# Optimization experiments

Hardware: AMD Instinct MI355X
Metric: run time of the kernel (lower is better)

The kernel has to match this reference:

```python
import jax, jax.numpy as jnp
import numpy as np

TAU = 0.05
EPS = 1e-5
NHEAD = 4

def _ln(x, s, b):
    m = jnp.mean(x, -1, keepdims=True)
    v = jnp.mean((x - m) ** 2, -1, keepdims=True)
    return (x - m) * jax.lax.rsqrt(v + EPS) * s + b

def _encoder(z, mask, w_qkv, b_qkv, w_o, b_o, w_ff1, b_ff1, w_ff2, b_ff2, ln1_s, ln1_b, ln2_s, ln2_b):
    # z: [B,L,D], mask: [B,L] bool, True = padded (masked out of attention)
    B, L, D = z.shape
    H = NHEAD
    hd = D // H
    scale = 1.0 / float(np.sqrt(hd))
    nlayers = w_qkv.shape[0]
    for l in range(nlayers):
        qkv = z @ w_qkv[l].T + b_qkv[l]              # [B,L,3D]
        q, k, v = jnp.split(qkv, 3, axis=-1)
        q = q.reshape(B, L, H, hd).transpose(0, 2, 1, 3)  # [B,H,L,hd]
        k = k.reshape(B, L, H, hd).transpose(0, 2, 1, 3)
        v = v.reshape(B, L, H, hd).transpose(0, 2, 1, 3)
        scores = jnp.einsum('bhqd,bhkd->bhqk', q, k) * scale
        scores = jnp.where(mask[:, None, None, :], -1e9, scores)
        attn = jax.nn.softmax(scores, axis=-1)
        o = jnp.einsum('bhqk,bhkd->bhqd', attn, v).transpose(0, 2, 1, 3).reshape(B, L, D)
        z = _ln(z + o @ w_o[l].T + b_o[l], ln1_s[l], ln1_b[l])
        ff = jax.nn.relu(z @ w_ff1[l].T + b_ff1[l]) @ w_ff2[l].T + b_ff2[l]
        z = _ln(z + ff, ln2_s[l], ln2_b[l])
    return z

def _branch(x, mask, w0, b0, enc_p, w1, b1, w2, b2):
    base = x[..., None] * w0[:, 0] + b0          # Linear(1, latent) on [B,L,1]
    enc = _encoder(base, mask, *enc_p)
    h = jnp.mean(enc, axis=1)                    # mean over seq (incl. padded, as original)
    h = jnp.tanh(h @ w1.T + b1)
    return jnp.tanh(h @ w2.T + b2)


def setup_inputs() -> dict:
    key = jax.random.key(0)
    B, L, D, FF, NL, C = 256, 256, 128, 2048, 3, 3
    ks = jax.random.split(key, 16)
    w = lambda k, shape: jax.random.normal(k, shape, jnp.float32) * 0.02
    return {
        'x': jax.random.normal(ks[0], (B, L), jnp.float32),
        'x_pos': jax.random.normal(ks[1], (B, L), jnp.float32),
        'x_neg': jax.random.normal(ks[2], (B, L), jnp.float32),
        'mask': jnp.zeros((B, L), bool),
        'pos_mask': jnp.zeros((B, L), bool),
        'neg_mask': jnp.zeros((B, L), bool),
        'w0': w(ks[3], (D, 1)), 'b0': jnp.zeros((D,), jnp.float32),
        'w_qkv': w(ks[4], (NL, 3 * D, D)), 'b_qkv': jnp.zeros((NL, 3 * D), jnp.float32),
        'w_o': w(ks[5], (NL, D, D)), 'b_o': jnp.zeros((NL, D), jnp.float32),
        'w_ff1': w(ks[6], (NL, FF, D)), 'b_ff1': jnp.zeros((NL, FF), jnp.float32),
        'w_ff2': w(ks[7], (NL, D, FF)), 'b_ff2': jnp.zeros((NL, D), jnp.float32),
        'ln1_s': jnp.ones((NL, D), jnp.float32), 'ln1_b': jnp.zeros((NL, D), jnp.float32),
        'ln2_s': jnp.ones((NL, D), jnp.float32), 'ln2_b': jnp.zeros((NL, D), jnp.float32),
        'w1': w(ks[8], (D, D)), 'b1': jnp.zeros((D,), jnp.float32),
        'w2': w(ks[9], (D, D)), 'b2': jnp.zeros((D,), jnp.float32),
        'w3': w(ks[10], (C, D)), 'b3': jnp.zeros((C,), jnp.float32),
    }


def reference(x, x_pos, x_neg, mask, pos_mask, neg_mask, w0, b0, w_qkv, b_qkv, w_o, b_o,
              w_ff1, b_ff1, w_ff2, b_ff2, ln1_s, ln1_b, ln2_s, ln2_b, w1, b1, w2, b2, w3, b3):
    enc_p = (w_qkv, b_qkv, w_o, b_o, w_ff1, b_ff1, w_ff2, b_ff2, ln1_s, ln1_b, ln2_s, ln2_b)
    hb = _branch(x, mask, w0, b0, enc_p, w1, b1, w2, b2)        # [B,D]
    hp = _branch(x_pos, pos_mask, w0, b0, enc_p, w1, b1, w2, b2)
    hn = _branch(x_neg, neg_mask, w0, b0, enc_p, w1, b1, w2, b2)
    logits = jax.nn.softmax(hb @ w3.T + b3, axis=1)
    nb = hb / jnp.linalg.norm(hb, axis=1, keepdims=True)
    nps = hp / jnp.linalg.norm(hp, axis=1, keepdims=True)
    nns = hn / jnp.linalg.norm(hn, axis=1, keepdims=True)
    # InfoNCE: bottom_i = sum_j exp(<nb_i,np_j>/tau) + exp(<nb_i,nn_j>/tau)
    pos_sim = jnp.sum(nb * nps, axis=1) / TAU                   # diag of nb@nps.T
    S = jnp.concatenate([nb @ nps.T, nb @ nns.T], axis=1) / TAU  # [B,2B]
    loss = jnp.mean(jax.nn.logsumexp(S, axis=1) - pos_sim)
    return (nb, hp, hn, logits, loss)
```

## Files before the change

kernel.cpp:

```cpp
#include <hip/hip_runtime.h>
#include <stdint.h>

typedef unsigned short u16;
typedef unsigned int   u32;
typedef unsigned long long u64;
typedef __bf16 bf16x8 __attribute__((ext_vector_type(8)));
typedef __bf16 bf16x4t __attribute__((ext_vector_type(4)));
typedef float  f32x4  __attribute__((ext_vector_type(4)));

#define LN_EPS 1e-5f
#define LSEQ   256
#define DM     128
#define B3     768
#define MTOT   196608
#define NQKV   384
#define FFD    2048

__device__ __forceinline__ u16 f2bf(float f) {
  __bf16 h = (__bf16)f;
  return __builtin_bit_cast(u16, h);
}
__device__ __forceinline__ float bf2f(u16 h) {
  u32 u = ((u32)h) << 16;
  return __builtin_bit_cast(float, u);
}
__device__ __forceinline__ bf16x8 ld_bf8(const u16* p) {
  return __builtin_bit_cast(bf16x8, *(const uint4*)p);
}
__device__ __forceinline__ f32x4 mfma16(bf16x8 a, bf16x8 b, f32x4 c) {
  return __builtin_amdgcn_mfma_f32_16x16x32_bf16(a, b, c, 0, 0, 0);
}
__device__ __forceinline__ void gload16(const u16* g, u16* l) {
  __builtin_amdgcn_global_load_lds(
      (__attribute__((address_space(1))) void*)(uintptr_t)g,
      (__attribute__((address_space(3))) void*)(uintptr_t)l, 16, 0, 0);
}
__device__ __forceinline__ u64 pack4bf(float a, float b, float c, float d) {
  bf16x4t t;
  t[0] = (__bf16)a; t[1] = (__bf16)b; t[2] = (__bf16)c; t[3] = (__bf16)d;
  return __builtin_bit_cast(u64, t);
}

__global__ __launch_bounds__(256) void k_cvt(const float* src, u16* dst, int n8) {
  int gid = blockIdx.x * 256 + threadIdx.x;
  if (gid >= n8) return;
  const float* s = src + gid * 8;
  union { u16 o[8]; uint4 v; } t;
#pragma unroll
  for (int j = 0; j < 8; ++j) t.o[j] = f2bf(s[j]);
  *(uint4*)(dst + (size_t)gid * 8) = t.v;
}

__global__ __launch_bounds__(256) void k_embed(const float* x, const float* xp, const float* xn,
                                               const float* w0, const float* b0, u16* zb) {
  int gid = blockIdx.x * 256 + threadIdx.x;
  int row = gid >> 4;
  int oct = gid & 15;
  int br  = row >> 16;
  int loc = row & 65535;
  const float* xs = br == 0 ? x : (br == 1 ? xp : xn);
  float xv = xs[loc];
  int d0 = oct * 8;
  union { u16 o[8]; uint4 v; } t;
#pragma unroll
  for (int j = 0; j < 8; ++j) t.o[j] = f2bf(xv * w0[d0 + j] + b0[d0 + j]);
  *(uint4*)(zb + (size_t)row * DM + d0) = t.v;
}

__global__ __launch_bounds__(256) void k_qkv(const u16* zb, const u16* wt, const float* bias, u16* out) {
  __shared__ union {
    struct { u16 A[16384]; u16 B[16384]; } s;
    u16 bounce[128 * 136];
  } u;
  int tid = threadIdx.x;
  int m0 = blockIdx.x * 128;
  int n0 = blockIdx.y * 128;
#pragma unroll
  for (int p = 0; p < 8; ++p) {
    int row = p * 16 + (tid >> 4);
    int gs = (tid & 15) ^ (row & 7);
    gload16(wt + (u64)(n0 + row) * 128 + gs * 8, u.s.A + p * 2048 + tid * 8);
  }
#pragma unroll
  for (int p = 0; p < 8; ++p) {
    int row = p * 16 + (tid >> 4);
    int gs = (tid & 15) ^ (row & 7);
    gload16(zb + (u64)(m0 + row) * 128 + gs * 8, u.s.B + p * 2048 + tid * 8);
  }
  __syncthreads();

  int lane = tid & 63, wv = tid >> 6;
  int l15 = lane & 15, g = lane >> 4;
  int wn = wv & 1, wm = wv >> 1;
  f32x4 acc[4][4] = {};
#pragma unroll
  for (int ks = 0; ks < 4; ++ks) {
    bf16x8 a[4], b[4];
#pragma unroll
    for (int i = 0; i < 4; ++i) {
      int row = wn * 64 + i * 16 + l15;
      int gz = (ks * 4 + g) ^ (row & 7);
      a[i] = ld_bf8(u.s.A + row * 128 + gz * 8);
    }
#pragma unroll
    for (int j = 0; j < 4; ++j) {
      int row = wm * 64 + j * 16 + l15;
      int gz = (ks * 4 + g) ^ (row & 7);
      b[j] = ld_bf8(u.s.B + row * 128 + gz * 8);
    }
#pragma unroll
    for (int i = 0; i < 4; ++i)
#pragma unroll
      for (int j = 0; j < 4; ++j) acc[i][j] = mfma16(a[i], b[j], acc[i][j]);
  }
  float bv[4][4];
#pragma unroll
  for (int i = 0; i < 4; ++i)
    *(f32x4*)bv[i] = *(const f32x4*)(bias + n0 + wn * 64 + i * 16 + g * 4);
  __syncthreads();
#pragma unroll
  for (int i = 0; i < 4; ++i) {
    int nq = wn * 64 + i * 16 + g * 4;
#pragma unroll
    for (int j = 0; j < 4; ++j) {
      int m = wm * 64 + j * 16 + l15;
      u64 pk = pack4bf(acc[i][j][0] + bv[i][0], acc[i][j][1] + bv[i][1],
                       acc[i][j][2] + bv[i][2], acc[i][j][3] + bv[i][3]);
      *(u64*)(u.bounce + m * 136 + nq) = pk;
    }
  }
  __syncthreads();
  {
    int row = tid >> 1, half = tid & 1;
    const u16* src = u.bounce + row * 136 + half * 64;
    u16* dst = out + (u64)(m0 + row) * NQKV + n0 + half * 64;
#pragma unroll
    for (int q = 0; q < 8; ++q) *(uint4*)(dst + q * 8) = *(const uint4*)(src + q * 8);
  }
}

__global__ __launch_bounds__(256) void k_attn(const u16* qkv, const unsigned char* mk0,
                                              const unsigned char* mk1, const unsigned char* mk2,
                                              u16* attno) {
  __shared__ u16 VT[32 * 264];
  __shared__ u16 P[4][64 * 72];
  __shared__ float pen[256];
  int tid = threadIdx.x;
  int bh = blockIdx.x;
  int bb = bh >> 2, h = bh & 3;
  {
    int br = bb >> 8, loc = bb & 255;
    const unsigned char* mp = br == 0 ? mk0 : (br == 1 ? mk1 : mk2);
    pen[tid] = mp[loc * 256 + tid] ? -1e9f : 0.0f;
  }
  {
    const u16* vsrc = qkv + (u64)(bb * 256 + tid) * NQKV + 256 + h * 32;
    u16 tmp[32];
    *(uint4*)(tmp) = *(const uint4*)vsrc;
    *(uint4*)(tmp + 8) = *(const uint4*)(vsrc + 8);
    *(uint4*)(tmp + 16) = *(const uint4*)(vsrc + 16);
    *(uint4*)(tmp + 24) = *(const uint4*)(vsrc + 24);
#pragma unroll
    for (int d = 0; d < 32; ++d) VT[d * 264 + tid] = tmp[d];
  }
  __syncthreads();

  int lane = tid & 63, wv = tid >> 6;
  int l15 = lane & 15, g = lane >> 4;
  const float scale2 = 0.25503492149314874f;

  bf16x8 qf[4];
#pragma unroll
  for (int j = 0; j < 4; ++j)
    qf[j] = ld_bf8(qkv + (u64)(bb * 256 + wv * 64 + j * 16 + l15) * NQKV + h * 32 + g * 8);
  bf16x8 kf[16];
#pragma unroll
  for (int kb = 0; kb < 16; ++kb)
    kf[kb] = ld_bf8(qkv + (u64)(bb * 256 + kb * 16 + l15) * NQKV + 128 + h * 32 + g * 8);

  f32x4 accO[2][4] = {};
  float lpart[4] = {0.f, 0.f, 0.f, 0.f};
  u16* Pw = &P[wv][0];
  f32x4 zf = {0.f, 0.f, 0.f, 0.f};

#pragma unroll
  for (int t = 0; t < 4; ++t) {
    f32x4 pq[4];
#pragma unroll
    for (int i = 0; i < 4; ++i) pq[i] = *(const f32x4*)(pen + t * 64 + i * 16 + g * 4);
#pragma unroll
    for (int jq = 0; jq < 4; ++jq) {
      f32x4 s[4];
#pragma unroll
      for (int i = 0; i < 4; ++i) s[i] = mfma16(kf[t * 4 + i], qf[jq], zf);
#pragma unroll
      for (int i = 0; i < 4; ++i) {
        float p0 = __builtin_amdgcn_exp2f(fmaf(s[i][0], scale2, pq[i][0]));
        float p1 = __builtin_amdgcn_exp2f(fmaf(s[i][1], scale2, pq[i][1]));
        float p2 = __builtin_amdgcn_exp2f(fmaf(s[i][2], scale2, pq[i][2]));
        float p3 = __builtin_amdgcn_exp2f(fmaf(s[i][3], scale2, pq[i][3]));
        lpart[jq] += (p0 + p1) + (p2 + p3);
        *(u64*)(Pw + (jq * 16 + l15) * 72 + i * 16 + g * 4) = pack4bf(p0, p1, p2, p3);
      }
    }
#pragma unroll
    for (int ks = 0; ks < 2; ++ks) {
      bf16x8 va[2], pb[4];
#pragma unroll
      for (int i = 0; i < 2; ++i)
        va[i] = ld_bf8(VT + (i * 16 + l15) * 264 + t * 64 + ks * 32 + g * 8);
#pragma unroll
      for (int jq = 0; jq < 4; ++jq)
        pb[jq] = ld_bf8(Pw + (jq * 16 + l15) * 72 + ks * 32 + g * 8);
#pragma unroll
      for (int i = 0; i < 2; ++i)
#pragma unroll
        for (int jq = 0; jq < 4; ++jq) accO[i][jq] = mfma16(va[i], pb[jq], accO[i][jq]);
    }
  }
#pragma unroll
  for (int jq = 0; jq < 4; ++jq) {
    float v = lpart[jq];
    v += __shfl_xor(v, 16);
    v += __shfl_xor(v, 32);
    lpart[jq] = 1.0f / v;
  }
#pragma unroll
  for (int i = 0; i < 2; ++i)
#pragma unroll
    for (int jq = 0; jq < 4; ++jq) {
      int q = wv * 64 + jq * 16 + l15;
      float li = lpart[jq];
      u64 pk = pack4bf(accO[i][jq][0] * li, accO[i][jq][1] * li,
                       accO[i][jq][2] * li, accO[i][jq][3] * li);
      *(u64*)(attno + ((u64)(bb * 4 + h) * 256 + q) * 32 + i * 16 + g * 4) = pk;
    }
}

__global__ __launch_bounds__(256) void k_oln(const u16* attno, const u16* wt, const float* bias,
                                             const float* lns, const float* lnb, u16* zb) {
  __shared__ union {
    struct { u16 A[16384]; u16 B[16384]; } s;
    float bounce[64 * 132];
  } u;
  int tid = threadIdx.x;
  int m0 = blockIdx.x * 128;
#pragma unroll
  for (int p = 0; p < 8; ++p) {
    int row = p * 16 + (tid >> 4);
    int gs = (tid & 15) ^ (row & 7);
    gload16(wt + (u64)row * 128 + gs * 8, u.s.A + p * 2048 + tid * 8);
  }
  int bb = m0 >> 8, lbase = m0 & 255;
#pragma unroll
  for (int p = 0; p < 8; ++p) {
    int row = p * 16 + (tid >> 4);
    int gs = (tid & 15) ^ (row & 7);
    int hh = gs >> 2, off = (gs & 3) * 8;
    gload16(attno + ((u64)(bb * 4 + hh) * 256 + lbase + row) * 32 + off,
            u.s.B + p * 2048 + tid * 8);
  }
  __syncthreads();

  int lane = tid & 63, wv = tid >> 6;
  int l15 = lane & 15, g = lane >> 4;
  int wn = wv & 1, wm = wv >> 1;
  f32x4 acc[4][4] = {};
#pragma unroll
  for (int ks = 0; ks < 4; ++ks) {
    bf16x8 a[4], b[4];
#pragma unroll
    for (int i = 0; i < 4; ++i) {
      int row = wn * 64 + i * 16 + l15;
      int gz = (ks * 4 + g) ^ (row & 7);
      a[i] = ld_bf8(u.s.A + row * 128 + gz * 8);
    }
#pragma unroll
    for (int j = 0; j < 4; ++j) {
      int row = wm * 64 + j * 16 + l15;
      int gz = (ks * 4 + g) ^ (row & 7);
      b[j] = ld_bf8(u.s.B + row * 128 + gz * 8);
    }
#pragma unroll
    for (int i = 0; i < 4; ++i)
#pragma unroll
      for (int j = 0; j < 4; ++j) acc[i][j] = mfma16(a[i], b[j], acc[i][j]);
  }
  for (int ph = 0; ph < 2; ++ph) {
    __syncthreads();
    if (wm == ph) {
#pragma unroll
      for (int i = 0; i < 4; ++i)
#pragma unroll
        for (int j = 0; j < 4; ++j) {
          int ml = j * 16 + l15;
          int nq = wn * 64 + i * 16 + g * 4;
          *(f32x4*)(u.bounce + ml * 132 + nq) = acc[i][j];
        }
    }
    __syncthreads();
    {
      int ql = tid >> 2, q4 = tid & 3;
      int mrow = m0 + ph * 64 + ql;
      const u16* zrow = zb + (u64)mrow * 128 + q4 * 32;
      float v[32];
      float s = 0.f, s2 = 0.f;
#pragma unroll
      for (int c = 0; c < 32; ++c) {
        float val = u.bounce[ql * 132 + q4 * 32 + c] + bias[q4 * 32 + c] + bf2f(zrow[c]);
        v[c] = val; s += val; s2 += val * val;
      }
      s += __shfl_xor(s, 1);  s += __shfl_xor(s, 2);
      s2 += __shfl_xor(s2, 1); s2 += __shfl_xor(s2, 2);
      float mean = s * (1.0f / 128.0f);
      float var = s2 * (1.0f / 128.0f) - mean * mean;
      float rstd = rsqrtf(var + LN_EPS);
      union { u16 o[32]; uint4 q[4]; } t;
#pragma unroll
      for (int c = 0; c < 32; ++c)
        t.o[c] = f2bf((v[c] - mean) * rstd * lns[q4 * 32 + c] + lnb[q4 * 32 + c]);
      u16* dst = zb + (u64)mrow * 128 + q4 * 32;
#pragma unroll
      for (int q = 0; q < 4; ++q) *(uint4*)(dst + q * 8) = t.q[q];
    }
  }
}

__global__ __launch_bounds__(256, 2) void k_ffn(u16* zb, const u16* w1, const float* b1,
                                                const u16* w2, const float* b2,
                                                const float* lns, const float* lnb) {
  __shared__ u16 W1b[2][8192];
  __shared__ u16 W2b[2][8192];
  __shared__ u16 H1s[4][2048];
  int tid = threadIdx.x;
  int m0 = blockIdx.x * 128;
  int lane = tid & 63, wv = tid >> 6;
  int l15 = lane & 15, g = lane >> 4;
  int qb = m0 + wv * 32;

  bf16x8 az[2][4];
#pragma unroll
  for (int j = 0; j < 2; ++j)
#pragma unroll
    for (int ks = 0; ks < 4; ++ks)
      az[j][ks] = ld_bf8(zb + (u64)(qb + j * 16 + l15) * 128 + ks * 32 + g * 8);

  {
#pragma unroll
    for (int p = 0; p < 4; ++p) {
      int row = p * 16 + (tid >> 4);
      int gs = (tid & 15) ^ (row & 7);
      gload16(w1 + (u64)row * 128 + gs * 8, W1b[0] + p * 2048 + tid * 8);
    }
#pragma unroll
    for (int p = 0; p < 4; ++p) {
      int row = p * 32 + (tid >> 3);
      int gs = (tid & 7) ^ (row & 7);
      gload16(w2 + (u64)row * FFD + gs * 8, W2b[0] + p * 2048 + tid * 8);
    }
  }
  __syncthreads();

  f32x4 acc2[8][2] = {};
  char* Hw = (char*)&H1s[wv][0];

  for (int c = 0; c < 32; ++c) {
    int cur = c & 1;
    if (c < 31) {
      const u16* w1n = w1 + (u64)(c + 1) * 64 * 128;
      const u16* w2n = w2 + (u64)(c + 1) * 64;
      u16* d1 = W1b[cur ^ 1];
      u16* d2 = W2b[cur ^ 1];
#pragma unroll
      for (int p = 0; p < 4; ++p) {
        int row = p * 16 + (tid >> 4);
        int gs = (tid & 15) ^ (row & 7);
        gload16(w1n + (u64)row * 128 + gs * 8, d1 + p * 2048 + tid * 8);
      }
#pragma unroll
      for (int p = 0; p < 4; ++p) {
        int row = p * 32 + (tid >> 3);
        int gs = (tid & 7) ^ (row & 7);
        gload16(w2n + (u64)row * FFD + gs * 8, d2 + p * 2048 + tid * 8);
      }
    }
    const u16* W1c = W1b[cur];
    const u16* W2c = W2b[cur];

    f32x4 a1[4][2] = {};
#pragma unroll
    for (int ks = 0; ks < 4; ++ks) {
      bf16x8 af[4];
#pragma unroll
      for (int i = 0; i < 4; ++i) {
        int row = i * 16 + l15;
        int gz = (ks * 4 + g) ^ (row & 7);
        af[i] = ld_bf8(W1c + row * 128 + gz * 8);
      }
#pragma unroll
      for (int i = 0; i < 4; ++i)
#pragma unroll
        for (int j = 0; j < 2; ++j) a1[i][j] = mfma16(af[i], az[j][ks], a1[i][j]);
    }
#pragma unroll
    for (int i = 0; i < 4; ++i) {
      f32x4 bq = *(const f32x4*)(b1 + c * 64 + i * 16 + g * 4);
#pragma unroll
      for (int j = 0; j < 2; ++j) {
        int q = j * 16 + l15;
        float t0 = a1[i][j][0] + bq[0]; t0 = t0 > 0.f ? t0 : 0.f;
        float t1 = a1[i][j][1] + bq[1]; t1 = t1 > 0.f ? t1 : 0.f;
        float t2 = a1[i][j][2] + bq[2]; t2 = t2 > 0.f ? t2 : 0.f;
        float t3 = a1[i][j][3] + bq[3]; t3 = t3 > 0.f ? t3 : 0.f;
        int off = (q * 128 + i * 32 + g * 8) ^ ((q & 7) << 4);
        *(u64*)(Hw + off) = pack4bf(t0, t1, t2, t3);
      }
    }
#pragma unroll
    for (int ks = 0; ks < 2; ++ks) {
      bf16x8 pb[2];
#pragma unroll
      for (int j = 0; j < 2; ++j) {
        int q = j * 16 + l15;
        int off = (q * 128 + ks * 64 + g * 16) ^ ((q & 7) << 4);
        pb[j] = ld_bf8((const u16*)(Hw + off));
      }
#pragma unroll
      for (int i = 0; i < 8; ++i) {
        int row = i * 16 + l15;
        int gz = (ks * 4 + g) ^ (row & 7);
        bf16x8 wf = ld_bf8(W2c + row * 64 + gz * 8);
#pragma unroll
        for (int j = 0; j < 2; ++j) acc2[i][j] = mfma16(wf, pb[j], acc2[i][j]);
      }
    }
    __syncthreads();
  }

  float s[2] = {0.f, 0.f}, s2[2] = {0.f, 0.f};
#pragma unroll
  for (int i = 0; i < 8; ++i) {
    f32x4 bq = *(const f32x4*)(b2 + i * 16 + g * 4);
#pragma unroll
    for (int j = 0; j < 2; ++j) {
      int q = qb + j * 16 + l15;
      u64 zo = *(const u64*)(zb + (u64)q * 128 + i * 16 + g * 4);
#pragma unroll
      for (int r = 0; r < 4; ++r) {
        float val = acc2[i][j][r] + bq[r] + bf2f((u16)(zo >> (16 * r)));
        acc2[i][j][r] = val;
        s[j] += val; s2[j] += val * val;
      }
    }
  }
  float mval[2], rstd[2];
#pragma unroll
  for (int j = 0; j < 2; ++j) {
    float a = s[j], b = s2[j];
    a += __shfl_xor(a, 16); a += __shfl_xor(a, 32);
    b += __shfl_xor(b, 16); b += __shfl_xor(b, 32);
    float mean = a * (1.0f / 128.0f);
    float var = b * (1.0f / 128.0f) - mean * mean;
    mval[j] = mean;
    rstd[j] = rsqrtf(var + LN_EPS);
  }
#pragma unroll
  for (int i = 0; i < 8; ++i) {
    f32x4 ls = *(const f32x4*)(lns + i * 16 + g * 4);
    f32x4 lb = *(const f32x4*)(lnb + i * 16 + g * 4);
#pragma unroll
    for (int j = 0; j < 2; ++j) {
      int q = qb + j * 16 + l15;
      u64 pk = pack4bf((acc2[i][j][0] - mval[j]) * rstd[j] * ls[0] + lb[0],
                       (acc2[i][j][1] - mval[j]) * rstd[j] * ls[1] + lb[1],
                       (acc2[i][j][2] - mval[j]) * rstd[j] * ls[2] + lb[2],
                       (acc2[i][j][3] - mval[j]) * rstd[j] * ls[3] + lb[3]);
      *(u64*)(zb + (u64)q * 128 + i * 16 + g * 4) = pk;
    }
  }
}

__global__ __launch_bounds__(256) void k_mean(const u16* zb, float* h) {
  __shared__ float part[4][128];
  int tid = threadIdx.x, bb = blockIdx.x;
  int d2 = tid & 63, lg = tid >> 6;
  float s0 = 0.f, s1 = 0.f;
  for (int li = 0; li < 64; ++li) {
    int l = lg * 64 + li;
    u32 v = *(const u32*)(zb + (u64)(bb * 256 + l) * 128 + d2 * 2);
    s0 += bf2f((u16)(v & 0xffffu));
    s1 += bf2f((u16)(v >> 16));
  }
  part[lg][d2 * 2] = s0;
  part[lg][d2 * 2 + 1] = s1;
  __syncthreads();
  if (tid < 128) {
    float s = part[0][tid] + part[1][tid] + part[2][tid] + part[3][tid];
    h[bb * 128 + tid] = s * (1.0f / 256.0f);
  }
}

__global__ __launch_bounds__(128) void k_head(const float* h, const float* w1, const float* b1,
                                              const float* w2, const float* b2, float* h2) {
  __shared__ float r0[128], r1[128];
  int tid = threadIdx.x, bb = blockIdx.x;
  r0[tid] = h[bb * 128 + tid];
  __syncthreads();
  float s = b1[tid];
  const float* wr = w1 + tid * 128;
  for (int k = 0; k < 128; ++k) s += r0[k] * wr[k];
  r1[tid] = tanhf(s);
  __syncthreads();
  float s2 = b2[tid];
  const float* wr2 = w2 + tid * 128;
  for (int k = 0; k < 128; ++k) s2 += r1[k] * wr2[k];
  h2[bb * 128 + tid] = tanhf(s2);
}

__global__ __launch_bounds__(128) void k_finalize(const float* h2, const float* w3, const float* b3,
                                                  float* nrm, float* out) {
  __shared__ float row[128];
  __shared__ float red[2];
  __shared__ float lg[3];
  int tid = threadIdx.x, i = blockIdx.x;
  float v = h2[i * 128 + tid];
  row[tid] = v;
  float sq = v * v;
#pragma unroll
  for (int o = 32; o; o >>= 1) sq += __shfl_xor(sq, o);
  if ((tid & 63) == 0) red[tid >> 6] = sq;
  __syncthreads();
  float rinv = rsqrtf(red[0] + red[1]);
  float nv = v * rinv;
  nrm[i * 128 + tid] = nv;
  int br = i >> 8, loc = i & 255;
  if (br == 0)      out[loc * 128 + tid] = nv;
  else if (br == 1) out[32768 + loc * 128 + tid] = v;
  else              out[65536 + loc * 128 + tid] = v;
  if (br == 0) {
    if (tid < 3) {
      float s = b3[tid];
      const float* wr = w3 + tid * 128;
      for (int k = 0; k < 128; ++k) s += row[k] * wr[k];
      lg[tid] = s;
    }
    __syncthreads();
    if (tid == 0) {
      float m = fmaxf(lg[0], fmaxf(lg[1], lg[2]));
      float e0 = __expf(lg[0] - m), e1 = __expf(lg[1] - m), e2 = __expf(lg[2] - m);
      float si = 1.0f / (e0 + e1 + e2);
      out[98304 + loc * 3 + 0] = e0 * si;
      out[98304 + loc * 3 + 1] = e1 * si;
      out[98304 + loc * 3 + 2] = e2 * si;
    }
  }
}

__global__ __launch_bounds__(256) void k_infonce(const float* nrm, float* partial) {
  __shared__ float nbi[128];
  __shared__ float red[8];
  __shared__ float posv;
  int tid = threadIdx.x, i = blockIdx.x;
  if (tid < 128) nbi[tid] = nrm[i * 128 + tid];
  __syncthreads();
  const float* a = nrm + (u64)(256 + tid) * 128;
  const float* b = nrm + (u64)(512 + tid) * 128;
  float s1 = 0.f, s2 = 0.f;
  for (int k = 0; k < 128; ++k) { s1 += nbi[k] * a[k]; s2 += nbi[k] * b[k]; }
  s1 *= 20.0f; s2 *= 20.0f;
  if (tid == i) posv = s1;
  float m = fmaxf(s1, s2);
#pragma unroll
  for (int o = 32; o; o >>= 1) m = fmaxf(m, __shfl_xor(m, o));
  if ((tid & 63) == 0) red[tid >> 6] = m;
  __syncthreads();
  float M = fmaxf(fmaxf(red[0], red[1]), fmaxf(red[2], red[3]));
  float e = __expf(s1 - M) + __expf(s2 - M);
#pragma unroll
  for (int o = 32; o; o >>= 1) e += __shfl_xor(e, o);
  if ((tid & 63) == 0) red[4 + (tid >> 6)] = e;
  __syncthreads();
  if (tid == 0) {
    float S = red[4] + red[5] + red[6] + red[7];
    partial[i] = logf(S) + M - posv;
  }
}

__global__ __launch_bounds__(256) void k_loss(const float* partial, float* out) {
  int tid = threadIdx.x;
  float v = partial[tid];
#pragma unroll
  for (int o = 32; o; o >>= 1) v += __shfl_xor(v, o);
  __shared__ float red[4];
  if ((tid & 63) == 0) red[tid >> 6] = v;
  __syncthreads();
  if (tid == 0) out[99072] = (red[0] + red[1] + red[2] + red[3]) * (1.0f / 256.0f);
}

extern "C" void kernel_launch(void* const* d_in, const int* in_sizes, int n_in,
                              void* d_out, int out_size, void* d_ws, size_t ws_size,
                              hipStream_t stream) {
  const float* x   = (const float*)d_in[0];
  const float* xp  = (const float*)d_in[1];
  const float* xn  = (const float*)d_in[2];
  const unsigned char* mk0 = (const unsigned char*)d_in[3];
  const unsigned char* mk1 = (const unsigned char*)d_in[4];
  const unsigned char* mk2 = (const unsigned char*)d_in[5];
  const float* w0   = (const float*)d_in[6];
  const float* b0   = (const float*)d_in[7];
  const float* wqkv = (const float*)d_in[8];
  const float* bqkv = (const float*)d_in[9];
  const float* wo   = (const float*)d_in[10];
  const float* bo   = (const float*)d_in[11];
  const float* wf1  = (const float*)d_in[12];
  const float* bf1  = (const float*)d_in[13];
  const float* wf2  = (const float*)d_in[14];
  const float* bf2v = (const float*)d_in[15];
  const float* l1s  = (const float*)d_in[16];
  const float* l1b  = (const float*)d_in[17];
  const float* l2s  = (const float*)d_in[18];
  const float* l2b  = (const float*)d_in[19];
  const float* w1   = (const float*)d_in[20];
  const float* b1   = (const float*)d_in[21];
  const float* w2   = (const float*)d_in[22];
  const float* b2   = (const float*)d_in[23];
  const float* w3   = (const float*)d_in[24];
  const float* b3   = (const float*)d_in[25];
  float* out = (float*)d_out;

  char* ws = (char*)d_ws;
  u16* zb    = (u16*)ws; ws += (size_t)MTOT * 128 * 2;
  u16* qkv   = (u16*)ws; ws += (size_t)MTOT * 384 * 2;
  u16* attno = (u16*)ws; ws += (size_t)MTOT * 128 * 2;
  u16* wqb   = (u16*)ws; ws += (size_t)3 * 384 * 128 * 2;
  u16* wob   = (u16*)ws; ws += (size_t)3 * 128 * 128 * 2;
  u16* wf1b  = (u16*)ws; ws += (size_t)3 * 2048 * 128 * 2;
  u16* wf2b  = (u16*)ws; ws += (size_t)3 * 128 * 2048 * 2;
  float* hbuf = (float*)ws; ws += (size_t)768 * 128 * 4;
  float* h2   = (float*)ws; ws += (size_t)768 * 128 * 4;
  float* nrm  = (float*)ws; ws += (size_t)768 * 128 * 4;
  float* partial = (float*)ws;

  k_cvt<<<72, 256, 0, stream>>>(wqkv, wqb, 3 * 384 * 128 / 8);
  k_cvt<<<24, 256, 0, stream>>>(wo, wob, 3 * 128 * 128 / 8);
  k_cvt<<<384, 256, 0, stream>>>(wf1, wf1b, 3 * 2048 * 128 / 8);
  k_cvt<<<384, 256, 0, stream>>>(wf2, wf2b, 3 * 128 * 2048 / 8);
  k_embed<<<12288, 256, 0, stream>>>(x, xp, xn, w0, b0, zb);

  for (int l = 0; l < 3; ++l) {
    k_qkv<<<dim3(1536, 3), 256, 0, stream>>>(zb, wqb + (size_t)l * 384 * 128,
                                             bqkv + l * 384, qkv);
    k_attn<<<3072, 256, 0, stream>>>(qkv, mk0, mk1, mk2, attno);
    k_oln<<<1536, 256, 0, stream>>>(attno, wob + (size_t)l * 128 * 128, bo + l * 128,
                                    l1s + l * 128, l1b + l * 128, zb);
    k_ffn<<<1536, 256, 0, stream>>>(zb, wf1b + (size_t)l * 2048 * 128, bf1 + l * 2048,
                                    wf2b + (size_t)l * 128 * 2048, bf2v + l * 128,
                                    l2s + l * 128, l2b + l * 128);
  }
  k_mean<<<768, 256, 0, stream>>>(zb, hbuf);
  k_head<<<768, 128, 0, stream>>>(hbuf, w1, b1, w2, b2, h2);
  k_finalize<<<768, 128, 0, stream>>>(h2, w3, b3, nrm, out);
  k_infonce<<<256, 256, 0, stream>>>(nrm, partial);
  k_loss<<<1, 256, 0, stream>>>(partial, out);
}
```

Before: 1.263 ms.

## Double FFN block row tile to 256 and stream hidden chunks in halves

The fused FFN kernel now processes 256 rows per block (64 per wave) instead of 128, halving the grid. Each weight chunk loaded into shared memory is therefore reused across twice as many rows, which halves global and LDS weight traffic per row. The hidden activation is produced and consumed in two 32-wide halves so the per-wave LDS staging buffer still fits. The cost is more registers (doubled accumulators and z fragments) and possibly lower occupancy under launch_bounds(256,2), plus fewer blocks across the device.

```diff
diff --git a/kernel.cpp b/kernel.cpp
--- a/kernel.cpp
+++ b/kernel.cpp
@@ -333,14 +333,14 @@
   __shared__ u16 W2b[2][8192];
   __shared__ u16 H1s[4][2048];
   int tid = threadIdx.x;
-  int m0 = blockIdx.x * 128;
+  int m0 = blockIdx.x * 256;
   int lane = tid & 63, wv = tid >> 6;
   int l15 = lane & 15, g = lane >> 4;
-  int qb = m0 + wv * 32;
-
-  bf16x8 az[2][4];
-#pragma unroll
-  for (int j = 0; j < 2; ++j)
+  int qb = m0 + wv * 64;
+
+  bf16x8 az[4][4];
+#pragma unroll
+  for (int j = 0; j < 4; ++j)
 #pragma unroll
     for (int ks = 0; ks < 4; ++ks)
       az[j][ks] = ld_bf8(zb + (u64)(qb + j * 16 + l15) * 128 + ks * 32 + g * 8);
@@ -361,7 +361,7 @@
   }
   __syncthreads();
 
-  f32x4 acc2[8][2] = {};
+  f32x4 acc2[8][4] = {};
   char* Hw = (char*)&H1s[wv][0];
 
   for (int c = 0; c < 32; ++c) {
@@ -387,62 +387,56 @@
     const u16* W1c = W1b[cur];
     const u16* W2c = W2b[cur];
 
-    f32x4 a1[4][2] = {};
-#pragma unroll
-    for (int ks = 0; ks < 4; ++ks) {
-      bf16x8 af[4];
-#pragma unroll
-      for (int i = 0; i < 4; ++i) {
-        int row = i * 16 + l15;
-        int gz = (ks * 4 + g) ^ (row & 7);
-        af[i] = ld_bf8(W1c + row * 128 + gz * 8);
-      }
-#pragma unroll
-      for (int i = 0; i < 4; ++i)
-#pragma unroll
-        for (int j = 0; j < 2; ++j) a1[i][j] = mfma16(af[i], az[j][ks], a1[i][j]);
-    }
-#pragma unroll
-    for (int i = 0; i < 4; ++i) {
-      f32x4 bq = *(const f32x4*)(b1 + c * 64 + i * 16 + g * 4);
-#pragma unroll
-      for (int j = 0; j < 2; ++j) {
+#pragma unroll
+    for (int h = 0; h < 2; ++h) {
+#pragma unroll
+      for (int il = 0; il < 2; ++il) {
+        f32x4 a1[4] = {};
+#pragma unroll
+        for (int ks = 0; ks < 4; ++ks) {
+          int row = (2 * h + il) * 16 + l15;
+          int gz = (ks * 4 + g) ^ (row & 7);
+          bf16x8 af = ld_bf8(W1c + row * 128 + gz * 8);
+#pragma unroll
+          for (int j = 0; j < 4; ++j) a1[j] = mfma16(af, az[j][ks], a1[j]);
+        }
+        f32x4 bq = *(const f32x4*)(b1 + c * 64 + h * 32 + il * 16 + g * 4);
+#pragma unroll
+        for (int j = 0; j < 4; ++j) {
+          int q = j * 16 + l15;
+          float t0 = a1[j][0] + bq[0]; t0 = t0 > 0.f ? t0 : 0.f;
+          float t1 = a1[j][1] + bq[1]; t1 = t1 > 0.f ? t1 : 0.f;
+          float t2 = a1[j][2] + bq[2]; t2 = t2 > 0.f ? t2 : 0.f;
+          float t3 = a1[j][3] + bq[3]; t3 = t3 > 0.f ? t3 : 0.f;
+          int off = q * 64 + ((il * 32 + g * 8) ^ ((q & 3) << 4));
+          *(u64*)(Hw + off) = pack4bf(t0, t1, t2, t3);
+        }
+      }
+      bf16x8 pb[4];
+#pragma unroll
+      for (int j = 0; j < 4; ++j) {
         int q = j * 16 + l15;
-        float t0 = a1[i][j][0] + bq[0]; t0 = t0 > 0.f ? t0 : 0.f;
-        float t1 = a1[i][j][1] + bq[1]; t1 = t1 > 0.f ? t1 : 0.f;
-        float t2 = a1[i][j][2] + bq[2]; t2 = t2 > 0.f ? t2 : 0.f;
-        float t3 = a1[i][j][3] + bq[3]; t3 = t3 > 0.f ? t3 : 0.f;
-        int off = (q * 128 + i * 32 + g * 8) ^ ((q & 7) << 4);
-        *(u64*)(Hw + off) = pack4bf(t0, t1, t2, t3);
-      }
-    }
-#pragma unroll
-    for (int ks = 0; ks < 2; ++ks) {
-      bf16x8 pb[2];
-#pragma unroll
-      for (int j = 0; j < 2; ++j) {
-        int q = j * 16 + l15;
-        int off = (q * 128 + ks * 64 + g * 16) ^ ((q & 7) << 4);
+        int off = q * 64 + ((g * 16) ^ ((q & 3) << 4));
         pb[j] = ld_bf8((const u16*)(Hw + off));
       }
 #pragma unroll
       for (int i = 0; i < 8; ++i) {
         int row = i * 16 + l15;
-        int gz = (ks * 4 + g) ^ (row & 7);
+        int gz = (h * 4 + g) ^ (row & 7);
         bf16x8 wf = ld_bf8(W2c + row * 64 + gz * 8);
 #pragma unroll
-        for (int j = 0; j < 2; ++j) acc2[i][j] = mfma16(wf, pb[j], acc2[i][j]);
+        for (int j = 0; j < 4; ++j) acc2[i][j] = mfma16(wf, pb[j], acc2[i][j]);
       }
     }
     __syncthreads();
   }
 
-  float s[2] = {0.f, 0.f}, s2[2] = {0.f, 0.f};
+  float s[4] = {0.f, 0.f, 0.f, 0.f}, s2[4] = {0.f, 0.f, 0.f, 0.f};
 #pragma unroll
   for (int i = 0; i < 8; ++i) {
     f32x4 bq = *(const f32x4*)(b2 + i * 16 + g * 4);
 #pragma unroll
-    for (int j = 0; j < 2; ++j) {
+    for (int j = 0; j < 4; ++j) {
       int q = qb + j * 16 + l15;
       u64 zo = *(const u64*)(zb + (u64)q * 128 + i * 16 + g * 4);
 #pragma unroll
@@ -453,9 +447,9 @@
       }
     }
   }
-  float mval[2], rstd[2];
-#pragma unroll
-  for (int j = 0; j < 2; ++j) {
+  float mval[4], rstd[4];
+#pragma unroll
+  for (int j = 0; j < 4; ++j) {
     float a = s[j], b = s2[j];
     a += __shfl_xor(a, 16); a += __shfl_xor(a, 32);
     b += __shfl_xor(b, 16); b += __shfl_xor(b, 32);
@@ -469,7 +463,7 @@
     f32x4 ls = *(const f32x4*)(lns + i * 16 + g * 4);
     f32x4 lb = *(const f32x4*)(lnb + i * 16 + g * 4);
 #pragma unroll
-    for (int j = 0; j < 2; ++j) {
+    for (int j = 0; j < 4; ++j) {
       int q = qb + j * 16 + l15;
       u64 pk = pack4bf((acc2[i][j][0] - mval[j]) * rstd[j] * ls[0] + lb[0],
                        (acc2[i][j][1] - mval[j]) * rstd[j] * ls[1] + lb[1],
@@ -653,9 +647,9 @@
     k_attn<<<3072, 256, 0, stream>>>(qkv, mk0, mk1, mk2, attno);
     k_oln<<<1536, 256, 0, stream>>>(attno, wob + (size_t)l * 128 * 128, bo + l * 128,
                                     l1s + l * 128, l1b + l * 128, zb);
-    k_ffn<<<1536, 256, 0, stream>>>(zb, wf1b + (size_t)l * 2048 * 128, bf1 + l * 2048,
-                                    wf2b + (size_t)l * 128 * 2048, bf2v + l * 128,
-                                    l2s + l * 128, l2b + l * 128);
+    k_ffn<<<768, 256, 0, stream>>>(zb, wf1b + (size_t)l * 2048 * 128, bf1 + l * 2048,
+                                   wf2b + (size_t)l * 128 * 2048, bf2v + l * 128,
+                                   l2s + l * 128, l2b + l * 128);
   }
   k_mean<<<768, 256, 0, stream>>>(zb, hbuf);
   k_head<<<768, 128, 0, stream>>>(hbuf, w1, b1, w2, b2, h2);
```

New measurement: 1.370 ms. +8.5%, slower.

## Software-pipeline FFN so next chunk's GEMM1 overlaps current chunk's GEMM2

Applied to the files above, without the earlier changes.

Restructures the FFN chunk loop. The first-layer GEMM for chunk c+1 is computed while the second-layer GEMM consumes chunk c's hidden activations, which sit in registers before being written to shared memory. W1 is prefetched two chunks ahead and W2 one chunk ahead, and a prologue computes chunk 0's hidden tile. The launch bound drops the minimum of two blocks per SM, which frees registers for the extra live state but may lower occupancy.

```diff
diff --git a/kernel.cpp b/kernel.cpp
--- a/kernel.cpp
+++ b/kernel.cpp
@@ -326,9 +326,9 @@
   }
 }
 
-__global__ __launch_bounds__(256, 2) void k_ffn(u16* zb, const u16* w1, const float* b1,
-                                                const u16* w2, const float* b2,
-                                                const float* lns, const float* lnb) {
+__global__ __launch_bounds__(256) void k_ffn(u16* zb, const u16* w1, const float* b1,
+                                             const u16* w2, const float* b2,
+                                             const float* lns, const float* lnb) {
   __shared__ u16 W1b[2][8192];
   __shared__ u16 W2b[2][8192];
   __shared__ u16 H1s[4][2048];
@@ -345,48 +345,29 @@
     for (int ks = 0; ks < 4; ++ks)
       az[j][ks] = ld_bf8(zb + (u64)(qb + j * 16 + l15) * 128 + ks * 32 + g * 8);
 
+  char* Hw = (char*)&H1s[wv][0];
+
+#pragma unroll
+  for (int p = 0; p < 4; ++p) {
+    int row = p * 16 + (tid >> 4);
+    int gs = (tid & 15) ^ (row & 7);
+    gload16(w1 + (u64)row * 128 + gs * 8, W1b[0] + p * 2048 + tid * 8);
+  }
+#pragma unroll
+  for (int p = 0; p < 4; ++p) {
+    int row = p * 32 + (tid >> 3);
+    int gs = (tid & 7) ^ (row & 7);
+    gload16(w2 + (u64)row * FFD + gs * 8, W2b[0] + p * 2048 + tid * 8);
+  }
+  __syncthreads();
+
   {
 #pragma unroll
     for (int p = 0; p < 4; ++p) {
       int row = p * 16 + (tid >> 4);
       int gs = (tid & 15) ^ (row & 7);
-      gload16(w1 + (u64)row * 128 + gs * 8, W1b[0] + p * 2048 + tid * 8);
-    }
-#pragma unroll
-    for (int p = 0; p < 4; ++p) {
-      int row = p * 32 + (tid >> 3);
-      int gs = (tid & 7) ^ (row & 7);
-      gload16(w2 + (u64)row * FFD + gs * 8, W2b[0] + p * 2048 + tid * 8);
-    }
-  }
-  __syncthreads();
-
-  f32x4 acc2[8][2] = {};
-  char* Hw = (char*)&H1s[wv][0];
-
-  for (int c = 0; c < 32; ++c) {
-    int cur = c & 1;
-    if (c < 31) {
-      const u16* w1n = w1 + (u64)(c + 1) * 64 * 128;
-      const u16* w2n = w2 + (u64)(c + 1) * 64;
-      u16* d1 = W1b[cur ^ 1];
-      u16* d2 = W2b[cur ^ 1];
-#pragma unroll
-      for (int p = 0; p < 4; ++p) {
-        int row = p * 16 + (tid >> 4);
-        int gs = (tid & 15) ^ (row & 7);
-        gload16(w1n + (u64)row * 128 + gs * 8, d1 + p * 2048 + tid * 8);
-      }
-#pragma unroll
-      for (int p = 0; p < 4; ++p) {
-        int row = p * 32 + (tid >> 3);
-        int gs = (tid & 7) ^ (row & 7);
-        gload16(w2n + (u64)row * FFD + gs * 8, d2 + p * 2048 + tid * 8);
-      }
-    }
-    const u16* W1c = W1b[cur];
-    const u16* W2c = W2b[cur];
-
+      gload16(w1 + (u64)(64 * 128) + (u64)row * 128 + gs * 8, W1b[1] + p * 2048 + tid * 8);
+    }
     f32x4 a1[4][2] = {};
 #pragma unroll
     for (int ks = 0; ks < 4; ++ks) {
@@ -395,7 +376,7 @@
       for (int i = 0; i < 4; ++i) {
         int row = i * 16 + l15;
         int gz = (ks * 4 + g) ^ (row & 7);
-        af[i] = ld_bf8(W1c + row * 128 + gz * 8);
+        af[i] = ld_bf8(W1b[0] + row * 128 + gz * 8);
       }
 #pragma unroll
       for (int i = 0; i < 4; ++i)
@@ -404,7 +385,7 @@
     }
 #pragma unroll
     for (int i = 0; i < 4; ++i) {
-      f32x4 bq = *(const f32x4*)(b1 + c * 64 + i * 16 + g * 4);
+      f32x4 bq = *(const f32x4*)(b1 + i * 16 + g * 4);
 #pragma unroll
       for (int j = 0; j < 2; ++j) {
         int q = j * 16 + l15;
@@ -416,22 +397,93 @@
         *(u64*)(Hw + off) = pack4bf(t0, t1, t2, t3);
       }
     }
-#pragma unroll
-    for (int ks = 0; ks < 2; ++ks) {
-      bf16x8 pb[2];
+  }
+  __syncthreads();
+
+  f32x4 acc2[8][2] = {};
+
+  for (int c = 0; c < 32; ++c) {
+    int cur = c & 1;
+    if (c < 30) {
+      const u16* w1n = w1 + (u64)(c + 2) * 64 * 128;
+      u16* d1 = W1b[cur];
+#pragma unroll
+      for (int p = 0; p < 4; ++p) {
+        int row = p * 16 + (tid >> 4);
+        int gs = (tid & 15) ^ (row & 7);
+        gload16(w1n + (u64)row * 128 + gs * 8, d1 + p * 2048 + tid * 8);
+      }
+    }
+    if (c < 31) {
+      const u16* w2n = w2 + (u64)(c + 1) * 64;
+      u16* d2 = W2b[cur ^ 1];
+#pragma unroll
+      for (int p = 0; p < 4; ++p) {
+        int row = p * 32 + (tid >> 3);
+        int gs = (tid & 7) ^ (row & 7);
+        gload16(w2n + (u64)row * FFD + gs * 8, d2 + p * 2048 + tid * 8);
+      }
+    }
+    u64 hp[4][2];
+    if (c < 31) {
+      f32x4 a1[4][2] = {};
+      const u16* W1c = W1b[cur ^ 1];
+#pragma unroll
+      for (int ks = 0; ks < 4; ++ks) {
+        bf16x8 af[4];
+#pragma unroll
+        for (int i = 0; i < 4; ++i) {
+          int row = i * 16 + l15;
+          int gz = (ks * 4 + g) ^ (row & 7);
+          af[i] = ld_bf8(W1c + row * 128 + gz * 8);
+        }
+#pragma unroll
+        for (int i = 0; i < 4; ++i)
+#pragma unroll
+          for (int j = 0; j < 2; ++j) a1[i][j] = mfma16(af[i], az[j][ks], a1[i][j]);
+      }
+#pragma unroll
+      for (int i = 0; i < 4; ++i) {
+        f32x4 bq = *(const f32x4*)(b1 + (c + 1) * 64 + i * 16 + g * 4);
+#pragma unroll
+        for (int j = 0; j < 2; ++j) {
+          float t0 = a1[i][j][0] + bq[0]; t0 = t0 > 0.f ? t0 : 0.f;
+          float t1 = a1[i][j][1] + bq[1]; t1 = t1 > 0.f ? t1 : 0.f;
+          float t2 = a1[i][j][2] + bq[2]; t2 = t2 > 0.f ? t2 : 0.f;
+          float t3 = a1[i][j][3] + bq[3]; t3 = t3 > 0.f ? t3 : 0.f;
+          hp[i][j] = pack4bf(t0, t1, t2, t3);
+        }
+      }
+    }
+    bf16x8 pb2[2][2];
+#pragma unroll
+    for (int ks = 0; ks < 2; ++ks)
 #pragma unroll
       for (int j = 0; j < 2; ++j) {
         int q = j * 16 + l15;
         int off = (q * 128 + ks * 64 + g * 16) ^ ((q & 7) << 4);
-        pb[j] = ld_bf8((const u16*)(Hw + off));
-      }
+        pb2[ks][j] = ld_bf8((const u16*)(Hw + off));
+      }
+    if (c < 31) {
+#pragma unroll
+      for (int i = 0; i < 4; ++i)
+#pragma unroll
+        for (int j = 0; j < 2; ++j) {
+          int q = j * 16 + l15;
+          int off = (q * 128 + i * 32 + g * 8) ^ ((q & 7) << 4);
+          *(u64*)(Hw + off) = hp[i][j];
+        }
+    }
+    const u16* W2c = W2b[cur];
+#pragma unroll
+    for (int ks = 0; ks < 2; ++ks) {
 #pragma unroll
       for (int i = 0; i < 8; ++i) {
         int row = i * 16 + l15;
         int gz = (ks * 4 + g) ^ (row & 7);
         bf16x8 wf = ld_bf8(W2c + row * 64 + gz * 8);
 #pragma unroll
-        for (int j = 0; j < 2; ++j) acc2[i][j] = mfma16(wf, pb[j], acc2[i][j]);
+        for (int j = 0; j < 2; ++j) acc2[i][j] = mfma16(wf, pb2[ks][j], acc2[i][j]);
       }
     }
     __syncthreads();
```

New measurement: 1.345 ms. 1.07x slower.
